# Optimization experiments

Measured on AMD Instinct MI355X. Metric: run time of the kernel, lower is better.

Reference implementation:

```python
import jax, jax.numpy as jnp
import numpy as np

N = 500000
D = 256
B = 4096

def setup_inputs() -> dict:
    key = jax.random.key(0)
    k1, k2, k3, k4 = jax.random.split(key, 4)
    x = jax.random.normal(k1, (N, D), dtype=jnp.float32)
    batch = jnp.sort(jax.random.randint(k2, (N,), 0, B))
    w = jax.random.normal(k3, (D,), dtype=jnp.float32) / np.sqrt(D)
    b = jax.random.normal(k4, (), dtype=jnp.float32) * 0.01
    return {"x": x, "w": w, "b": b, "batch": batch, "num_segments": B}

def reference(x, w, b, batch, num_segments):
    # gate_nn: Linear(num_features, 1) -> squeeze(-1)
    scores = x @ w + b                                   # [N]
    # scatter_softmax over segments (numerically stable)
    seg_max = jax.ops.segment_max(scores, batch, num_segments=num_segments)  # [B]
    shifted = scores - seg_max[batch]
    e = jnp.exp(shifted)                                 # [N]
    denom = jax.ops.segment_sum(e, batch, num_segments=num_segments)         # [B]
    attn = e / denom[batch]                              # [N]
    # scatter_sum of attention-weighted features
    out = jax.ops.segment_sum(x * attn[:, None], batch, num_segments=num_segments)  # [B, D]
    return out
```

## Files before the change

kernel.cpp:

```cpp
#include <hip/hip_runtime.h>
#include <math.h>

#define D 256
#define BLOCK 256
#define NWAVES 4
#define R 4

__global__ __launch_bounds__(BLOCK) void niche_attn_kernel(
    const float* __restrict__ x,
    const float* __restrict__ w,
    const float* __restrict__ bptr,
    const int*   __restrict__ batch,
    float*       __restrict__ out,
    int N)
{
    const int seg  = blockIdx.x;
    const int tid  = threadIdx.x;
    const int wave = tid >> 6;
    const int lane = tid & 63;

    __shared__ int   s_bounds[2];
    __shared__ float s_m[NWAVES];
    __shared__ float s_l[NWAVES];
    __shared__ float s_acc[NWAVES][D];

    if (tid < 2) {
        const int target = seg + tid;
        int lo = 0, hi = N;
        while (lo < hi) {
            const int mid = (lo + hi) >> 1;
            if (batch[mid] < target) lo = mid + 1; else hi = mid;
        }
        s_bounds[tid] = lo;
    }
    __syncthreads();
    const int row_start = s_bounds[0];
    const int row_end   = s_bounds[1];

    float* outp = out + (size_t)seg * D;

    if (row_end <= row_start) {
        outp[tid] = 0.f;
        return;
    }

    const int    col  = lane << 2;
    const float4 w4   = *(const float4*)(w + col);
    const float  bias = *bptr;

    float  m = -INFINITY;
    float  l = 0.f;
    float4 acc = make_float4(0.f, 0.f, 0.f, 0.f);

    const int step = NWAVES * R;
    int row = row_start + wave * R;

    float4 cx[R];
    if (row < row_end) {
#pragma unroll
        for (int i = 0; i < R; ++i) {
            int r = row + i; r = (r < row_end) ? r : (row_end - 1);
            cx[i] = *(const float4*)(x + (size_t)r * D + col);
        }
    }

    while (row < row_end) {
        const int nrow = row + step;
        float4 nx[R];
#pragma unroll
        for (int i = 0; i < R; ++i) {
            int r = nrow + i; r = (r < row_end) ? r : (row_end - 1);
            nx[i] = *(const float4*)(x + (size_t)r * D + col);
        }

        float s[R];
#pragma unroll
        for (int i = 0; i < R; ++i)
            s[i] = cx[i].x * w4.x + cx[i].y * w4.y + cx[i].z * w4.z + cx[i].w * w4.w;
#pragma unroll
        for (int off = 32; off > 0; off >>= 1) {
#pragma unroll
            for (int i = 0; i < R; ++i)
                s[i] += __shfl_xor(s[i], off, 64);
        }
#pragma unroll
        for (int i = 0; i < R; ++i)
            s[i] = (row + i < row_end) ? (s[i] + bias) : -INFINITY;

        const float cmax = fmaxf(fmaxf(s[0], s[1]), fmaxf(s[2], s[3]));
        const float newm = fmaxf(m, cmax);
        const float alpha = __expf(m - newm);
        float p[R];
#pragma unroll
        for (int i = 0; i < R; ++i)
            p[i] = __expf(s[i] - newm);

        l = l * alpha + ((p[0] + p[1]) + (p[2] + p[3]));
        acc.x *= alpha; acc.y *= alpha; acc.z *= alpha; acc.w *= alpha;
#pragma unroll
        for (int i = 0; i < R; ++i) {
            acc.x = fmaf(cx[i].x, p[i], acc.x);
            acc.y = fmaf(cx[i].y, p[i], acc.y);
            acc.z = fmaf(cx[i].z, p[i], acc.z);
            acc.w = fmaf(cx[i].w, p[i], acc.w);
        }
        m = newm;

#pragma unroll
        for (int i = 0; i < R; ++i) cx[i] = nx[i];
        row = nrow;
    }

    if (lane == 0) { s_m[wave] = m; s_l[wave] = l; }
    __syncthreads();

    const float M = fmaxf(fmaxf(s_m[0], s_m[1]), fmaxf(s_m[2], s_m[3]));
    float L = 0.f;
#pragma unroll
    for (int wv = 0; wv < NWAVES; ++wv)
        L += s_l[wv] * __expf(s_m[wv] - M);

    const float scale = __expf(m - M);
    s_acc[wave][col + 0] = acc.x * scale;
    s_acc[wave][col + 1] = acc.y * scale;
    s_acc[wave][col + 2] = acc.z * scale;
    s_acc[wave][col + 3] = acc.w * scale;
    __syncthreads();

    const float invL = 1.f / L;
    const float v = (s_acc[0][tid] + s_acc[1][tid]) + (s_acc[2][tid] + s_acc[3][tid]);
    outp[tid] = v * invL;
}

extern "C" void kernel_launch(void* const* d_in, const int* in_sizes, int n_in,
                              void* d_out, int out_size, void* d_ws, size_t ws_size,
                              hipStream_t stream)
{
    const float* x     = (const float*)d_in[0];
    const float* w     = (const float*)d_in[1];
    const float* b     = (const float*)d_in[2];
    const int*   batch = (const int*)d_in[3];
    float*       out   = (float*)d_out;

    const int N = in_sizes[3];
    const int B = out_size / D;

    niche_attn_kernel<<<B, BLOCK, 0, stream>>>(x, w, b, batch, out, N);
}
```

Before: 658.7 us.

## Precompute segment starts in separate kernel, use nontemporal loads and ping-pong buffers

Replaces the per-block binary search over batch with a preceding kernel that writes segment start offsets to workspace, which removes a serial chain of dependent global loads at the head of every block. The x stream now uses nontemporal loads, the prefetch loop is restructured into an A/B ping-pong so register copies disappear, and launch bounds request 4 blocks per CU. The cost is an extra kernel launch plus a full pass over batch, and the change depends on workspace being large enough for B+1 ints.

```diff
diff --git a/kernel.cpp b/kernel.cpp
--- a/kernel.cpp
+++ b/kernel.cpp
@@ -6,36 +6,40 @@
 #define NWAVES 4
 #define R 4
 
-__global__ __launch_bounds__(BLOCK) void niche_attn_kernel(
+typedef float f32x4 __attribute__((ext_vector_type(4)));
+
+__global__ void seg_bounds_kernel(const int* __restrict__ batch,
+                                  int* __restrict__ starts, int N, int B)
+{
+    int i = blockIdx.x * blockDim.x + threadIdx.x;
+    const int stride = gridDim.x * blockDim.x;
+    for (; i < N; i += stride) {
+        const int cur  = batch[i];
+        const int prev = (i == 0) ? -1 : batch[i - 1];
+        for (int s = prev + 1; s <= cur; ++s) starts[s] = i;
+        if (i == N - 1)
+            for (int s = cur + 1; s <= B; ++s) starts[s] = N;
+    }
+}
+
+__global__ __launch_bounds__(BLOCK, 4) void niche_attn_kernel(
     const float* __restrict__ x,
     const float* __restrict__ w,
     const float* __restrict__ bptr,
-    const int*   __restrict__ batch,
-    float*       __restrict__ out,
-    int N)
+    const int*   __restrict__ starts,
+    float*       __restrict__ out)
 {
     const int seg  = blockIdx.x;
     const int tid  = threadIdx.x;
     const int wave = tid >> 6;
     const int lane = tid & 63;
 
-    __shared__ int   s_bounds[2];
     __shared__ float s_m[NWAVES];
     __shared__ float s_l[NWAVES];
     __shared__ float s_acc[NWAVES][D];
 
-    if (tid < 2) {
-        const int target = seg + tid;
-        int lo = 0, hi = N;
-        while (lo < hi) {
-            const int mid = (lo + hi) >> 1;
-            if (batch[mid] < target) lo = mid + 1; else hi = mid;
-        }
-        s_bounds[tid] = lo;
-    }
-    __syncthreads();
-    const int row_start = s_bounds[0];
-    const int row_end   = s_bounds[1];
+    const int row_start = starts[seg];
+    const int row_end   = starts[seg + 1];
 
     float* outp = out + (size_t)seg * D;
 
@@ -44,39 +48,34 @@
         return;
     }
 
-    const int    col  = lane << 2;
-    const float4 w4   = *(const float4*)(w + col);
-    const float  bias = *bptr;
+    const int   col  = lane << 2;
+    const f32x4 w4   = *(const f32x4*)(w + col);
+    const float bias = *bptr;
 
-    float  m = -INFINITY;
-    float  l = 0.f;
-    float4 acc = make_float4(0.f, 0.f, 0.f, 0.f);
+    float m = -INFINITY;
+    float l = 0.f;
+    f32x4 acc = {0.f, 0.f, 0.f, 0.f};
 
     const int step = NWAVES * R;
     int row = row_start + wave * R;
 
-    float4 cx[R];
-    if (row < row_end) {
+    f32x4 bufA[R], bufB[R];
+
+    auto loadc = [&](f32x4* buf, int r0) {
 #pragma unroll
         for (int i = 0; i < R; ++i) {
-            int r = row + i; r = (r < row_end) ? r : (row_end - 1);
-            cx[i] = *(const float4*)(x + (size_t)r * D + col);
+            int r = r0 + i; r = (r < row_end) ? r : (row_end - 1);
+            buf[i] = __builtin_nontemporal_load(
+                         (const f32x4*)(x + (size_t)r * D + col));
         }
-    }
+    };
 
-    while (row < row_end) {
-        const int nrow = row + step;
-        float4 nx[R];
-#pragma unroll
-        for (int i = 0; i < R; ++i) {
-            int r = nrow + i; r = (r < row_end) ? r : (row_end - 1);
-            nx[i] = *(const float4*)(x + (size_t)r * D + col);
-        }
-
+    auto compute = [&](const f32x4* buf, int r0) {
         float s[R];
 #pragma unroll
         for (int i = 0; i < R; ++i)
-            s[i] = cx[i].x * w4.x + cx[i].y * w4.y + cx[i].z * w4.z + cx[i].w * w4.w;
+            s[i] = buf[i].x * w4.x + buf[i].y * w4.y
+                 + buf[i].z * w4.z + buf[i].w * w4.w;
 #pragma unroll
         for (int off = 32; off > 0; off >>= 1) {
 #pragma unroll
@@ -85,7 +84,7 @@
         }
 #pragma unroll
         for (int i = 0; i < R; ++i)
-            s[i] = (row + i < row_end) ? (s[i] + bias) : -INFINITY;
+            s[i] = (r0 + i < row_end) ? (s[i] + bias) : -INFINITY;
 
         const float cmax = fmaxf(fmaxf(s[0], s[1]), fmaxf(s[2], s[3]));
         const float newm = fmaxf(m, cmax);
@@ -99,15 +98,24 @@
         acc.x *= alpha; acc.y *= alpha; acc.z *= alpha; acc.w *= alpha;
 #pragma unroll
         for (int i = 0; i < R; ++i) {
-            acc.x = fmaf(cx[i].x, p[i], acc.x);
-            acc.y = fmaf(cx[i].y, p[i], acc.y);
-            acc.z = fmaf(cx[i].z, p[i], acc.z);
-            acc.w = fmaf(cx[i].w, p[i], acc.w);
+            acc.x = fmaf(buf[i].x, p[i], acc.x);
+            acc.y = fmaf(buf[i].y, p[i], acc.y);
+            acc.z = fmaf(buf[i].z, p[i], acc.z);
+            acc.w = fmaf(buf[i].w, p[i], acc.w);
         }
         m = newm;
+    };
 
-#pragma unroll
-        for (int i = 0; i < R; ++i) cx[i] = nx[i];
+    if (row < row_end) loadc(bufA, row);
+    while (row < row_end) {
+        int nrow = row + step;
+        loadc(bufB, nrow);
+        compute(bufA, row);
+        row = nrow;
+        if (row >= row_end) break;
+        nrow = row + step;
+        loadc(bufA, nrow);
+        compute(bufB, row);
         row = nrow;
     }
 
@@ -141,9 +149,11 @@
     const float* b     = (const float*)d_in[2];
     const int*   batch = (const int*)d_in[3];
     float*       out   = (float*)d_out;
+    int*         starts = (int*)d_ws;
 
     const int N = in_sizes[3];
     const int B = out_size / D;
 
-    niche_attn_kernel<<<B, BLOCK, 0, stream>>>(x, w, b, batch, out, N);
+    seg_bounds_kernel<<<1024, BLOCK, 0, stream>>>(batch, starts, N, B);
+    niche_attn_kernel<<<B, BLOCK, 0, stream>>>(x, w, b, starts, out);
 }
```

New measurement: 622.7 us. -5.5%, faster.
